# Performance work log

Measured on AMD Instinct MI355X. Metric: run time of the kernel, lower is better.

Reference implementation:

```python
import jax, jax.numpy as jnp
import numpy as np

N_NODES = 50000
N_EDGES = 1600000
N_FEAT = 256
HDIM = 64
HEADS = 8
N_GRAPHS = 64
NEG_SLOPE = 0.2


def gat_layer(x, src, dst, W, a_src, a_dst, b, heads, out_c, concat):
    # x: [N, F]; W: [F, heads*out_c]; a_src/a_dst: [heads, out_c]; b: bias
    N = x.shape[0]
    h = (x @ W).reshape(N, heads, out_c)              # [N, H, C]
    alpha_s = jnp.sum(h * a_src, axis=-1)             # [N, H]
    alpha_d = jnp.sum(h * a_dst, axis=-1)             # [N, H]
    e = jax.nn.leaky_relu(alpha_s[src] + alpha_d[dst], NEG_SLOPE)  # [E, H]
    # numerically stable segment softmax over incoming edges of each dst node
    m = jax.lax.stop_gradient(jax.ops.segment_max(e, dst, num_segments=N))
    p = jnp.exp(e - m[dst])
    denom = jax.ops.segment_sum(p, dst, num_segments=N)
    alpha = p / denom[dst]                            # [E, H]
    out = jax.ops.segment_sum(h[src] * alpha[:, :, None], dst, num_segments=N)  # [N, H, C]
    out = out.reshape(N, heads * out_c) if concat else out.mean(axis=1)
    return out + b


def setup_inputs() -> dict:
    key = jax.random.key(0)
    ks = jax.random.split(key, 10)
    x = jax.random.normal(ks[0], (N_NODES, N_FEAT), dtype=jnp.float32)
    edge_index = jax.random.randint(ks[1], (2, N_EDGES), 0, N_NODES, dtype=jnp.int64)
    batch = jnp.sort(jax.random.randint(ks[2], (N_NODES,), 0, N_GRAPHS, dtype=jnp.int64))
    c1 = HDIM // HEADS  # 8 channels per head
    s1 = 1.0 / np.sqrt(N_FEAT)
    s2 = 1.0 / np.sqrt(HDIM)
    W1 = jax.random.normal(ks[3], (N_FEAT, HEADS * c1), dtype=jnp.float32) * s1
    a_src1 = jax.random.normal(ks[4], (HEADS, c1), dtype=jnp.float32) * s2
    a_dst1 = jax.random.normal(ks[5], (HEADS, c1), dtype=jnp.float32) * s2
    b1 = jnp.zeros((HEADS * c1,), dtype=jnp.float32)
    W2 = jax.random.normal(ks[6], (HDIM, 1), dtype=jnp.float32) * s2
    a_src2 = jax.random.normal(ks[7], (1, 1), dtype=jnp.float32)
    a_dst2 = jax.random.normal(ks[8], (1, 1), dtype=jnp.float32)
    b2 = jnp.zeros((1,), dtype=jnp.float32)
    return {"x": x, "edge_index": edge_index, "batch": batch,
            "W1": W1, "a_src1": a_src1, "a_dst1": a_dst1, "b1": b1,
            "W2": W2, "a_src2": a_src2, "a_dst2": a_dst2, "b2": b2}


def reference(x, edge_index, batch, W1, a_src1, a_dst1, b1, W2, a_src2, a_dst2, b2):
    N = x.shape[0]
    # PyG GATConv adds self-loops by default
    loops = jnp.arange(N, dtype=edge_index.dtype)
    src = jnp.concatenate([edge_index[0], loops])
    dst = jnp.concatenate([edge_index[1], loops])
    c1 = HDIM // HEADS
    h = gat_layer(x, src, dst, W1, a_src1, a_dst1, b1, HEADS, c1, concat=True)
    h = jax.nn.relu(h)
    # dropout is identity in eval mode (training=False)
    h = gat_layer(h, src, dst, W2, a_src2, a_dst2, b2, 1, 1, concat=False)  # [N, 1]
    # global mean pool over graphs
    counts = jax.ops.segment_sum(jnp.ones((N,), dtype=h.dtype), batch, num_segments=N_GRAPHS)
    sums = jax.ops.segment_sum(h, batch, num_segments=N_GRAPHS)  # [G, 1]
    return sums / jnp.maximum(counts, 1.0)[:, None]
```

## Files before the change

### kernel.cpp

```cpp
#include <hip/hip_runtime.h>
#include <hip/hip_bf16.h>
#include <hip/hip_fp16.h>
#include <math.h>

#define NF 256
#define NO 64
#define NHEAD 8
#define NEG_SLOPE 0.2f
#define BM 64
#define KB 64
#define LS 68
#define BKT 128
#define NBLK 256
#define RCAP 8192

__device__ __forceinline__ float lrelu(float x) { return x > 0.f ? x : NEG_SLOPE * x; }

__global__ __launch_bounds__(256) void k_front(
    const float* __restrict__ x, const float* __restrict__ W,
    const float* __restrict__ a_src, const float* __restrict__ a_dst,
    __half* __restrict__ h1h, float* __restrict__ as1, float* __restrict__ ad1,
    const int* __restrict__ eidx, unsigned* __restrict__ M,
    float* __restrict__ gacc, int N, int E, int GB, int NB, int CH)
{
    __shared__ float xl[BM][LS];
    __shared__ float wl[KB][LS];

    if (blockIdx.x >= GB) {
        unsigned* hist = (unsigned*)&xl[0][0];
        for (int i = threadIdx.x; i < NB; i += 256) hist[i] = 0;
        __syncthreads();
        const int blk = blockIdx.x - GB;
        const int lo = blk * CH;
        const int hi = min(lo + CH, E + N);
        for (int i = lo + (int)threadIdx.x; i < hi; i += 256) {
            int d = (i < E) ? eidx[E + i] : (i - E);
            atomicAdd(&hist[d >> 7], 1u);
        }
        __syncthreads();
        for (int b = threadIdx.x; b < NB; b += 256)
            M[(size_t)b * NBLK + blk] = hist[b];
        return;
    }

    if (blockIdx.x == 0) {
        for (int i = threadIdx.x; i < 1024; i += 256) gacc[i] = 0.f;
    }
    const int t  = threadIdx.x;
    const int tx = t & 15;
    const int ty = t >> 4;
    const int row0 = blockIdx.x * BM;

    float acc[4][4] = {};

    for (int kc = 0; kc < NF; kc += KB) {
        #pragma unroll
        for (int i = 0; i < 4; ++i) {
            int r = (t >> 4) + 16 * i;
            int row = row0 + r; if (row >= N) row = N - 1;
            float4 v = *(const float4*)(x + (size_t)row * NF + kc + 4 * tx);
            *(float4*)&xl[r][4 * tx] = v;
        }
        #pragma unroll
        for (int i = 0; i < 4; ++i) {
            int k = (t >> 4) + 16 * i;
            float4 v = *(const float4*)(W + (size_t)(kc + k) * NO + 4 * tx);
            *(float4*)&wl[k][4 * tx] = v;
        }
        __syncthreads();

        #pragma unroll
        for (int k = 0; k < KB; k += 4) {
            float4 xv[4], wv[4];
            #pragma unroll
            for (int r = 0; r < 4; ++r)
                xv[r] = *(const float4*)&xl[4 * ty + r][k];
            #pragma unroll
            for (int kk = 0; kk < 4; ++kk)
                wv[kk] = *(const float4*)&wl[k + kk][4 * tx];
            #pragma unroll
            for (int r = 0; r < 4; ++r) {
                float4 xr = xv[r];
                #pragma unroll
                for (int kk = 0; kk < 4; ++kk) {
                    float xk = (kk == 0) ? xr.x : (kk == 1) ? xr.y : (kk == 2) ? xr.z : xr.w;
                    acc[r][0] = fmaf(xk, wv[kk].x, acc[r][0]);
                    acc[r][1] = fmaf(xk, wv[kk].y, acc[r][1]);
                    acc[r][2] = fmaf(xk, wv[kk].z, acc[r][2]);
                    acc[r][3] = fmaf(xk, wv[kk].w, acc[r][3]);
                }
            }
        }
        __syncthreads();
    }

    const float4 avs = *(const float4*)(a_src + 4 * tx);
    const float4 avd = *(const float4*)(a_dst + 4 * tx);
    #pragma unroll
    for (int r = 0; r < 4; ++r) {
        int row = row0 + 4 * ty + r;
        if (row >= N) continue;
        float4 o = make_float4(acc[r][0], acc[r][1], acc[r][2], acc[r][3]);
        __half2 p0 = __float22half2_rn(make_float2(o.x, o.y));
        __half2 p1 = __float22half2_rn(make_float2(o.z, o.w));
        __half2* dst2 = (__half2*)(h1h + (size_t)row * NO + 4 * tx);
        dst2[0] = p0;
        dst2[1] = p1;
        float vs = o.x * avs.x + o.y * avs.y + o.z * avs.z + o.w * avs.w;
        float vd = o.x * avd.x + o.y * avd.y + o.z * avd.z + o.w * avd.w;
        vs += __shfl_xor(vs, 1);
        vd += __shfl_xor(vd, 1);
        if ((tx & 1) == 0) {
            as1[row * NHEAD + (tx >> 1)] = vs;
            ad1[row * NHEAD + (tx >> 1)] = vd;
        }
    }
}

__global__ __launch_bounds__(1024) void k_scan2(
    unsigned* __restrict__ M, unsigned* __restrict__ Bbase, int NB)
{
    __shared__ unsigned tot[512];
    __shared__ unsigned basel[513];
    const int t = threadIdx.x, lane = t & 63, w = t >> 6;

    for (int b = w; b < NB; b += 16) {
        uint4 v = ((const uint4*)&M[(size_t)b * NBLK])[lane];
        unsigned s = v.x + v.y + v.z + v.w;
        #pragma unroll
        for (int m = 1; m < 64; m <<= 1) s += __shfl_xor(s, m);
        if (lane == 0) tot[b] = s;
    }
    __syncthreads();
    if (t == 0) {
        unsigned r = 0;
        for (int b = 0; b < NB; ++b) { basel[b] = r; r += tot[b]; }
        basel[NB] = r;
    }
    __syncthreads();
    for (int b = t; b <= NB; b += 1024) Bbase[b] = basel[b];
    for (int b = w; b < NB; b += 16) {
        uint4 v = ((const uint4*)&M[(size_t)b * NBLK])[lane];
        unsigned lsum = v.x + v.y + v.z + v.w;
        unsigned p = lsum;
        #pragma unroll
        for (int d = 1; d < 64; d <<= 1) {
            unsigned q = __shfl_up(p, d);
            if (lane >= d) p += q;
        }
        unsigned c0 = basel[b] + p - lsum;
        uint4 o;
        o.x = c0;
        o.y = c0 + v.x;
        o.z = o.y + v.y;
        o.w = o.z + v.z;
        ((uint4*)&M[(size_t)b * NBLK])[lane] = o;
    }
}

__global__ __launch_bounds__(256) void k_bscatter(
    const int* __restrict__ eidx, int E, int N, int NB, int CH,
    const unsigned* __restrict__ M, unsigned* __restrict__ rbuf)
{
    __shared__ unsigned cur[512];
    const int blk = blockIdx.x;
    for (int b = threadIdx.x; b < NB; b += 256)
        cur[b] = M[(size_t)b * NBLK + blk];
    __syncthreads();
    const int lo = blk * CH;
    const int hi = min(lo + CH, E + N);
    for (int i = lo + (int)threadIdx.x; i < hi; i += 256) {
        int s, d;
        if (i < E) { s = eidx[i]; d = eidx[E + i]; }
        else       { s = i - E;   d = i - E; }
        unsigned pos = atomicAdd(&cur[d >> 7], 1u);
        rbuf[pos] = ((unsigned)s << 7) | (unsigned)(d & (BKT - 1));
    }
}

__global__ __launch_bounds__(256) void k_csr(
    const unsigned* __restrict__ Bbase, int N, int NB,
    unsigned* __restrict__ rbuf, unsigned* __restrict__ offs)
{
    __shared__ unsigned recs[RCAP];
    __shared__ unsigned nhist[BKT];
    __shared__ unsigned ncur[BKT];
    __shared__ unsigned wtotS;
    const int b = blockIdx.x;
    const unsigned base = Bbase[b], end = Bbase[b + 1];
    const int cnt = (int)(end - base);
    const int nodes = min(BKT, N - b * BKT);

    for (int i = threadIdx.x; i < BKT; i += 256) nhist[i] = 0;
    __syncthreads();
    for (int i = threadIdx.x; i < cnt; i += 256) {
        unsigned r = rbuf[base + i];
        recs[i] = r;
        atomicAdd(&nhist[r & (BKT - 1)], 1u);
    }
    __syncthreads();
    const int tl = threadIdx.x & 127;
    unsigned v = nhist[tl], p = v;
    #pragma unroll
    for (int d = 1; d < 64; d <<= 1) {
        unsigned q = __shfl_up(p, d);
        if ((tl & 63) >= d) p += q;
    }
    if (threadIdx.x == 63) wtotS = p;
    __syncthreads();
    unsigned excl = base + ((tl >= 64) ? wtotS : 0u) + p - v;
    if (threadIdx.x < 128) {
        ncur[tl] = excl;
        if (tl < nodes) offs[b * BKT + tl] = excl;
    }
    if (b == NB - 1 && threadIdx.x == 0) offs[N] = end;
    __syncthreads();
    for (int i = threadIdx.x; i < cnt; i += 256) {
        unsigned r = recs[i];
        unsigned pos = atomicAdd(&ncur[r & (BKT - 1)], 1u);
        rbuf[pos] = r >> 7;
    }
}

__global__ __launch_bounds__(256) void k_gat1(
    const unsigned* __restrict__ offs, const int* __restrict__ csr,
    const float4* __restrict__ h1q,
    const float* __restrict__ as1, const float* __restrict__ ad1,
    const float* __restrict__ b1, const float* __restrict__ W2,
    float* __restrict__ h2, int N)
{
    const int lane = threadIdx.x & 63;
    const int n = blockIdx.x * (blockDim.x >> 6) + (threadIdx.x >> 6);
    if (n >= N) return;
    const int slot = lane >> 3;
    const int head = lane & 7;
    const unsigned s0 = offs[n];
    const unsigned deg = offs[n + 1] - s0;
    const float ad = ad1[n * NHEAD + head];

    float acc[8] = {};
    float den = 0.f;

    unsigned k = (unsigned)slot;
    for (; k + 24 < deg; k += 32) {
        int sA = csr[s0 + k],      sB = csr[s0 + k + 8];
        int sC = csr[s0 + k + 16], sD = csr[s0 + k + 24];
        float aA = as1[sA * NHEAD + head], aB = as1[sB * NHEAD + head];
        float aC = as1[sC * NHEAD + head], aD = as1[sD * NHEAD + head];
        float4 rA = h1q[(unsigned)sA * 8u + head];
        float4 rB = h1q[(unsigned)sB * 8u + head];
        float4 rC = h1q[(unsigned)sC * 8u + head];
        float4 rD = h1q[(unsigned)sD * 8u + head];
        float pA = __expf(lrelu(aA + ad));
        float pB = __expf(lrelu(aB + ad));
        float pC = __expf(lrelu(aC + ad));
        float pD = __expf(lrelu(aD + ad));
        den += (pA + pB) + (pC + pD);
        const __half2* hA = (const __half2*)&rA;
        const __half2* hB = (const __half2*)&rB;
        const __half2* hC = (const __half2*)&rC;
        const __half2* hD = (const __half2*)&rD;
        #pragma unroll
        for (int j = 0; j < 4; ++j) {
            float2 fA = __half22float2(hA[j]);
            float2 fB = __half22float2(hB[j]);
            float2 fC = __half22float2(hC[j]);
            float2 fD = __half22float2(hD[j]);
            acc[2 * j]     = fmaf(pA, fA.x, acc[2 * j]);
            acc[2 * j + 1] = fmaf(pA, fA.y, acc[2 * j + 1]);
            acc[2 * j]     = fmaf(pB, fB.x, acc[2 * j]);
            acc[2 * j + 1] = fmaf(pB, fB.y, acc[2 * j + 1]);
            acc[2 * j]     = fmaf(pC, fC.x, acc[2 * j]);
            acc[2 * j + 1] = fmaf(pC, fC.y, acc[2 * j + 1]);
            acc[2 * j]     = fmaf(pD, fD.x, acc[2 * j]);
            acc[2 * j + 1] = fmaf(pD, fD.y, acc[2 * j + 1]);
        }
    }
    for (; k + 8 < deg; k += 16) {
        int sA = csr[s0 + k], sB = csr[s0 + k + 8];
        float aA = as1[sA * NHEAD + head], aB = as1[sB * NHEAD + head];
        float4 rA = h1q[(unsigned)sA * 8u + head];
        float4 rB = h1q[(unsigned)sB * 8u + head];
        float pA = __expf(lrelu(aA + ad));
        float pB = __expf(lrelu(aB + ad));
        den += pA + pB;
        const __half2* hA = (const __half2*)&rA;
        const __half2* hB = (const __half2*)&rB;
        #pragma unroll
        for (int j = 0; j < 4; ++j) {
            float2 fA = __half22float2(hA[j]);
            float2 fB = __half22float2(hB[j]);
            acc[2 * j]     = fmaf(pA, fA.x, acc[2 * j]);
            acc[2 * j + 1] = fmaf(pA, fA.y, acc[2 * j + 1]);
            acc[2 * j]     = fmaf(pB, fB.x, acc[2 * j]);
            acc[2 * j + 1] = fmaf(pB, fB.y, acc[2 * j + 1]);
        }
    }
    if (k < deg) {
        int s = csr[s0 + k];
        float a = as1[s * NHEAD + head];
        float4 r = h1q[(unsigned)s * 8u + head];
        float p = __expf(lrelu(a + ad));
        den += p;
        const __half2* hh = (const __half2*)&r;
        #pragma unroll
        for (int j = 0; j < 4; ++j) {
            float2 f = __half22float2(hh[j]);
            acc[2 * j]     = fmaf(p, f.x, acc[2 * j]);
            acc[2 * j + 1] = fmaf(p, f.y, acc[2 * j + 1]);
        }
    }

    #pragma unroll
    for (int r = 0; r < 8; ++r) {
        acc[r] += __shfl_xor(acc[r], 8);
        acc[r] += __shfl_xor(acc[r], 16);
        acc[r] += __shfl_xor(acc[r], 32);
    }
    den += __shfl_xor(den, 8);
    den += __shfl_xor(den, 16);
    den += __shfl_xor(den, 32);

    const float4 b0 = ((const float4*)b1)[head * 2];
    const float4 b1v = ((const float4*)b1)[head * 2 + 1];
    const float4 w0 = ((const float4*)W2)[head * 2];
    const float4 w1v = ((const float4*)W2)[head * 2 + 1];
    const float inv = 1.f / den;
    float tt = 0.f;
    tt += fmaxf(fmaf(acc[0], inv, b0.x), 0.f) * w0.x;
    tt += fmaxf(fmaf(acc[1], inv, b0.y), 0.f) * w0.y;
    tt += fmaxf(fmaf(acc[2], inv, b0.z), 0.f) * w0.z;
    tt += fmaxf(fmaf(acc[3], inv, b0.w), 0.f) * w0.w;
    tt += fmaxf(fmaf(acc[4], inv, b1v.x), 0.f) * w1v.x;
    tt += fmaxf(fmaf(acc[5], inv, b1v.y), 0.f) * w1v.y;
    tt += fmaxf(fmaf(acc[6], inv, b1v.z), 0.f) * w1v.z;
    tt += fmaxf(fmaf(acc[7], inv, b1v.w), 0.f) * w1v.w;
    tt += __shfl_xor(tt, 1);
    tt += __shfl_xor(tt, 2);
    tt += __shfl_xor(tt, 4);
    if (lane == 0) h2[n] = tt;
}

__global__ __launch_bounds__(1024) void k_gat2pool(
    const unsigned* __restrict__ offs, const int* __restrict__ csr,
    const float* __restrict__ h2, const int* __restrict__ batch,
    const float* __restrict__ a_src2, const float* __restrict__ a_dst2,
    const float* __restrict__ b2, float* __restrict__ gacc, int N)
{
    __shared__ float vals[64];
    __shared__ int gid[64];
    const int t = threadIdx.x;
    if (t < 64) gid[t] = -1;
    __syncthreads();

    const int lane = t & 63;
    const int ql = lane & 15;
    const int slot = (t >> 6) * 4 + (lane >> 4);
    const int n = blockIdx.x * 64 + slot;

    if (n < N) {
        const float aS = a_src2[0], aD = a_dst2[0];
        const unsigned s0 = offs[n], s1 = offs[n + 1];
        const float ad = h2[n] * aD;
        float num = 0.f, den = 0.f;
        for (unsigned j = s0 + (unsigned)ql; j < s1; j += 16) {
            float hs = h2[csr[j]];
            float p = __expf(lrelu(hs * aS + ad));
            num = fmaf(p, hs, num);
            den += p;
        }
        #pragma unroll
        for (int msk = 1; msk < 16; msk <<= 1) {
            num += __shfl_xor(num, msk);
            den += __shfl_xor(den, msk);
        }
        if (ql == 0) {
            vals[slot] = num / den + b2[0];
            gid[slot] = batch[n];
        }
    }
    __syncthreads();

    if (t < 64) {
        int g = gid[t];
        float o = (g >= 0) ? vals[t] : 0.f;
        const int g0 = __shfl(g, 0);
        const bool same = (g == g0);
        float s = same ? o : 0.f;
        float c = (same && g >= 0) ? 1.f : 0.f;
        #pragma unroll
        for (int msk = 1; msk < 64; msk <<= 1) {
            s += __shfl_xor(s, msk);
            c += __shfl_xor(c, msk);
        }
        if (t == 0) {
            unsafeAtomicAdd(&gacc[g0 * 16], s);
            unsafeAtomicAdd(&gacc[g0 * 16 + 1], c);
        }
        if (g >= 0 && !same) {
            unsafeAtomicAdd(&gacc[g * 16], o);
            unsafeAtomicAdd(&gacc[g * 16 + 1], 1.0f);
        }
    }
}

__global__ void k_final(const float* __restrict__ gacc,
                        float* __restrict__ out, int G)
{
    int g = blockIdx.x * blockDim.x + threadIdx.x;
    if (g < G) out[g] = gacc[g * 16] / fmaxf(gacc[g * 16 + 1], 1.0f);
}

extern "C" void kernel_launch(void* const* d_in, const int* in_sizes, int n_in,
                              void* d_out, int out_size, void* d_ws, size_t ws_size,
                              hipStream_t stream)
{
    const float* x      = (const float*)d_in[0];
    const int*   eidx   = (const int*)d_in[1];
    const int*   batch  = (const int*)d_in[2];
    const float* W1     = (const float*)d_in[3];
    const float* a_src1 = (const float*)d_in[4];
    const float* a_dst1 = (const float*)d_in[5];
    const float* b1     = (const float*)d_in[6];
    const float* W2     = (const float*)d_in[7];
    const float* a_src2 = (const float*)d_in[8];
    const float* a_dst2 = (const float*)d_in[9];
    const float* b2     = (const float*)d_in[10];

    const int N = in_sizes[0] / NF;
    const int E = in_sizes[1] / 2;
    const int G = out_size;
    const int ETOT = E + N;
    const int NB = (N + BKT - 1) / BKT;
    const int CH = (ETOT + NBLK - 1) / NBLK;
    const int GB = (N + BM - 1) / BM;

    char* w = (char*)d_ws;
    __half*   h1h   = (__half*)(w + 0);
    float*    as1   = (float*)(w + 6400000);
    float*    ad1   = (float*)(w + 8000000);
    float*    h2    = (float*)(w + 9600000);
    unsigned* offs  = (unsigned*)(w + 9800000);
    unsigned* rbuf  = (unsigned*)(w + 10000064);
    unsigned* M     = (unsigned*)(w + 16600064);
    unsigned* Bbase = (unsigned*)(w + 17000448);
    float*    gacc  = (float*)(w + 17002496);

    k_front<<<GB + NBLK, 256, 0, stream>>>(x, W1, a_src1, a_dst1,
                                           h1h, as1, ad1,
                                           eidx, M, gacc, N, E, GB, NB, CH);
    k_scan2<<<1, 1024, 0, stream>>>(M, Bbase, NB);
    k_bscatter<<<NBLK, 256, 0, stream>>>(eidx, E, N, NB, CH, M, rbuf);
    k_csr<<<NB, 256, 0, stream>>>(Bbase, N, NB, rbuf, offs);

    const int* csr = (const int*)rbuf;
    k_gat1<<<(N + 3) / 4, 256, 0, stream>>>(offs, csr, (const float4*)h1h,
                                            as1, ad1, b1, W2, h2, N);
    k_gat2pool<<<(N + 63) / 64, 1024, 0, stream>>>(offs, csr, h2, batch,
                                                   a_src2, a_dst2, b2, gacc, N);
    k_final<<<1, 64, 0, stream>>>(gacc, (float*)d_out, G);
}
```

Before: 145.2 us.

## Use fp16 packed dot2 GEMM with register-prefetched tiles in front kernel

The x@W projection now converts x and W tiles to packed fp16 pairs in shared memory and accumulates with the fdot2 instruction in fp32, halving LDS traffic and FMA count. Global loads for the next K chunk are prefetched into registers while the current chunk is staged, overlapping memory latency with compute. Rounding inputs to fp16 lowers GEMM precision. The histogram scratch also moves into its own shared array.

```diff
diff --git a/kernel.cpp b/kernel.cpp
--- a/kernel.cpp
+++ b/kernel.cpp
@@ -9,12 +9,27 @@
 #define NEG_SLOPE 0.2f
 #define BM 64
 #define KB 64
-#define LS 68
 #define BKT 128
 #define NBLK 256
 #define RCAP 8192
 
 __device__ __forceinline__ float lrelu(float x) { return x > 0.f ? x : NEG_SLOPE * x; }
+
+typedef _Float16 f16x2 __attribute__((ext_vector_type(2)));
+
+__device__ __forceinline__ unsigned f2u(float a, float b) {
+    return __builtin_bit_cast(unsigned, __float22half2_rn(make_float2(a, b)));
+}
+__device__ __forceinline__ float dot2f(unsigned a, unsigned b, float c) {
+#if __has_builtin(__builtin_amdgcn_fdot2)
+    return __builtin_amdgcn_fdot2(__builtin_bit_cast(f16x2, a),
+                                  __builtin_bit_cast(f16x2, b), c, false);
+#else
+    float2 fa = __half22float2(__builtin_bit_cast(__half2, a));
+    float2 fb = __half22float2(__builtin_bit_cast(__half2, b));
+    return fmaf(fa.x, fb.x, fmaf(fa.y, fb.y, c));
+#endif
+}
 
 __global__ __launch_bounds__(256) void k_front(
     const float* __restrict__ x, const float* __restrict__ W,
@@ -23,11 +38,11 @@
     const int* __restrict__ eidx, unsigned* __restrict__ M,
     float* __restrict__ gacc, int N, int E, int GB, int NB, int CH)
 {
-    __shared__ float xl[BM][LS];
-    __shared__ float wl[KB][LS];
+    __shared__ unsigned xl2[BM][36];
+    __shared__ unsigned wl2[KB / 2][68];
+    __shared__ unsigned hist[512];
 
     if (blockIdx.x >= GB) {
-        unsigned* hist = (unsigned*)&xl[0][0];
         for (int i = threadIdx.x; i < NB; i += 256) hist[i] = 0;
         __syncthreads();
         const int blk = blockIdx.x - GB;
@@ -52,46 +67,73 @@
     const int row0 = blockIdx.x * BM;
 
     float acc[4][4] = {};
+    float4 xr[4], wr[4];
+
+    #pragma unroll
+    for (int i = 0; i < 4; ++i) {
+        int row = row0 + ty + 16 * i; if (row >= N) row = N - 1;
+        xr[i] = *(const float4*)(x + (size_t)row * NF + 4 * tx);
+    }
+    #pragma unroll
+    for (int i = 0; i < 2; ++i) {
+        int p = ty + 16 * i;
+        wr[2 * i]     = *(const float4*)(W + (size_t)(2 * p) * NO + 4 * tx);
+        wr[2 * i + 1] = *(const float4*)(W + (size_t)(2 * p + 1) * NO + 4 * tx);
+    }
 
     for (int kc = 0; kc < NF; kc += KB) {
+        __syncthreads();
         #pragma unroll
         for (int i = 0; i < 4; ++i) {
-            int r = (t >> 4) + 16 * i;
-            int row = row0 + r; if (row >= N) row = N - 1;
-            float4 v = *(const float4*)(x + (size_t)row * NF + kc + 4 * tx);
-            *(float4*)&xl[r][4 * tx] = v;
-        }
-        #pragma unroll
-        for (int i = 0; i < 4; ++i) {
-            int k = (t >> 4) + 16 * i;
-            float4 v = *(const float4*)(W + (size_t)(kc + k) * NO + 4 * tx);
-            *(float4*)&wl[k][4 * tx] = v;
+            int r = ty + 16 * i;
+            *(uint2*)&xl2[r][2 * tx] =
+                make_uint2(f2u(xr[i].x, xr[i].y), f2u(xr[i].z, xr[i].w));
+        }
+        #pragma unroll
+        for (int i = 0; i < 2; ++i) {
+            int p = ty + 16 * i;
+            float4 lo = wr[2 * i], hi = wr[2 * i + 1];
+            *(uint4*)&wl2[p][4 * tx] =
+                make_uint4(f2u(lo.x, hi.x), f2u(lo.y, hi.y),
+                           f2u(lo.z, hi.z), f2u(lo.w, hi.w));
+        }
+        if (kc + KB < NF) {
+            const int kn = kc + KB;
+            #pragma unroll
+            for (int i = 0; i < 4; ++i) {
+                int row = row0 + ty + 16 * i; if (row >= N) row = N - 1;
+                xr[i] = *(const float4*)(x + (size_t)row * NF + kn + 4 * tx);
+            }
+            #pragma unroll
+            for (int i = 0; i < 2; ++i) {
+                int p = ty + 16 * i;
+                wr[2 * i]     = *(const float4*)(W + (size_t)(kn + 2 * p) * NO + 4 * tx);
+                wr[2 * i + 1] = *(const float4*)(W + (size_t)(kn + 2 * p + 1) * NO + 4 * tx);
+            }
         }
         __syncthreads();
-
-        #pragma unroll
-        for (int k = 0; k < KB; k += 4) {
-            float4 xv[4], wv[4];
+        #pragma unroll
+        for (int kk = 0; kk < KB / 2; kk += 4) {
+            uint4 xv[4], wv[4];
             #pragma unroll
             for (int r = 0; r < 4; ++r)
-                xv[r] = *(const float4*)&xl[4 * ty + r][k];
+                xv[r] = *(const uint4*)&xl2[4 * ty + r][kk];
             #pragma unroll
-            for (int kk = 0; kk < 4; ++kk)
-                wv[kk] = *(const float4*)&wl[k + kk][4 * tx];
+            for (int j = 0; j < 4; ++j)
+                wv[j] = *(const uint4*)&wl2[kk + j][4 * tx];
             #pragma unroll
             for (int r = 0; r < 4; ++r) {
-                float4 xr = xv[r];
                 #pragma unroll
-                for (int kk = 0; kk < 4; ++kk) {
-                    float xk = (kk == 0) ? xr.x : (kk == 1) ? xr.y : (kk == 2) ? xr.z : xr.w;
-                    acc[r][0] = fmaf(xk, wv[kk].x, acc[r][0]);
-                    acc[r][1] = fmaf(xk, wv[kk].y, acc[r][1]);
-                    acc[r][2] = fmaf(xk, wv[kk].z, acc[r][2]);
-                    acc[r][3] = fmaf(xk, wv[kk].w, acc[r][3]);
+                for (int j = 0; j < 4; ++j) {
+                    unsigned xa = (j == 0) ? xv[r].x : (j == 1) ? xv[r].y
+                                : (j == 2) ? xv[r].z : xv[r].w;
+                    acc[r][0] = dot2f(xa, wv[j].x, acc[r][0]);
+                    acc[r][1] = dot2f(xa, wv[j].y, acc[r][1]);
+                    acc[r][2] = dot2f(xa, wv[j].z, acc[r][2]);
+                    acc[r][3] = dot2f(xa, wv[j].w, acc[r][3]);
                 }
             }
         }
-        __syncthreads();
     }
 
     const float4 avs = *(const float4*)(a_src + 4 * tx);
```

New measurement: 494.6 us. 241% more time.

## Compute first-layer projection with fp16 MFMA instead of fp32 FMA

Applied to the files above, without the earlier changes.

The x@W1 GEMM in k_front moves from a scalar fp32 register-tiled FMA loop to 16x16x32 f16 MFMA instructions. x and W are converted to packed half2 in shared memory, and W is stored transposed. The K tile grows to 128, and the epilogue computes the attention logits per head with lane shuffles over the MFMA output layout. The goal is to cut the GEMM's compute time, at the cost of fp16 input precision and scalar, non-vectorized stores of h1h.

```diff
diff --git a/kernel.cpp b/kernel.cpp
--- a/kernel.cpp
+++ b/kernel.cpp
@@ -7,14 +7,19 @@
 #define NO 64
 #define NHEAD 8
 #define NEG_SLOPE 0.2f
-#define BM 64
-#define KB 64
-#define LS 68
 #define BKT 128
 #define NBLK 256
 #define RCAP 8192
 
 __device__ __forceinline__ float lrelu(float x) { return x > 0.f ? x : NEG_SLOPE * x; }
+
+typedef _Float16 f16x8 __attribute__((ext_vector_type(8)));
+typedef float f32x4 __attribute__((ext_vector_type(4)));
+
+__device__ __forceinline__ unsigned f2u(float a, float b) {
+    __half2 h = __float22half2_rn(make_float2(a, b));
+    return *(unsigned*)&h;
+}
 
 __global__ __launch_bounds__(256) void k_front(
     const float* __restrict__ x, const float* __restrict__ W,
@@ -23,11 +28,11 @@
     const int* __restrict__ eidx, unsigned* __restrict__ M,
     float* __restrict__ gacc, int N, int E, int GB, int NB, int CH)
 {
-    __shared__ float xl[BM][LS];
-    __shared__ float wl[KB][LS];
+    __shared__ unsigned xl2[64][68];
+    __shared__ unsigned wl2[64][68];
 
     if (blockIdx.x >= GB) {
-        unsigned* hist = (unsigned*)&xl[0][0];
+        unsigned* hist = &xl2[0][0];
         for (int i = threadIdx.x; i < NB; i += 256) hist[i] = 0;
         __syncthreads();
         const int blk = blockIdx.x - GB;
@@ -46,73 +51,72 @@
     if (blockIdx.x == 0) {
         for (int i = threadIdx.x; i < 1024; i += 256) gacc[i] = 0.f;
     }
-    const int t  = threadIdx.x;
-    const int tx = t & 15;
-    const int ty = t >> 4;
-    const int row0 = blockIdx.x * BM;
-
-    float acc[4][4] = {};
-
-    for (int kc = 0; kc < NF; kc += KB) {
-        #pragma unroll
-        for (int i = 0; i < 4; ++i) {
-            int r = (t >> 4) + 16 * i;
+    const int t   = threadIdx.x;
+    const int lw  = t & 63;
+    const int wv  = t >> 6;
+    const int row0 = blockIdx.x * 64;
+
+    f32x4 acc[4] = {};
+
+    for (int kc = 0; kc < NF; kc += 128) {
+        if (kc) __syncthreads();
+        {
+            const int r = t >> 2, q = t & 3;
             int row = row0 + r; if (row >= N) row = N - 1;
-            float4 v = *(const float4*)(x + (size_t)row * NF + kc + 4 * tx);
-            *(float4*)&xl[r][4 * tx] = v;
-        }
-        #pragma unroll
-        for (int i = 0; i < 4; ++i) {
-            int k = (t >> 4) + 16 * i;
-            float4 v = *(const float4*)(W + (size_t)(kc + k) * NO + 4 * tx);
-            *(float4*)&wl[k][4 * tx] = v;
+            const float4* xs = (const float4*)(x + (size_t)row * NF + kc + q * 32);
+            #pragma unroll
+            for (int i = 0; i < 8; ++i) {
+                float4 v = xs[i];
+                xl2[r][q * 16 + 2 * i]     = f2u(v.x, v.y);
+                xl2[r][q * 16 + 2 * i + 1] = f2u(v.z, v.w);
+            }
+        }
+        {
+            const int c = t & 63, seg = t >> 6;
+            #pragma unroll
+            for (int m = 0; m < 16; ++m) {
+                int k = kc + seg * 32 + 2 * m;
+                float w0 = W[(size_t)k * NO + c];
+                float w1 = W[(size_t)(k + 1) * NO + c];
+                wl2[c][seg * 16 + m] = f2u(w0, w1);
+            }
         }
         __syncthreads();
 
-        #pragma unroll
-        for (int k = 0; k < KB; k += 4) {
-            float4 xv[4], wv[4];
+        const int mrow = 16 * wv + (lw & 15);
+        const int fcol = (lw >> 4) * 4;
+        #pragma unroll
+        for (int ks = 0; ks < 4; ++ks) {
+            f16x8 a = *(const f16x8*)&xl2[mrow][ks * 16 + fcol];
             #pragma unroll
-            for (int r = 0; r < 4; ++r)
-                xv[r] = *(const float4*)&xl[4 * ty + r][k];
-            #pragma unroll
-            for (int kk = 0; kk < 4; ++kk)
-                wv[kk] = *(const float4*)&wl[k + kk][4 * tx];
-            #pragma unroll
-            for (int r = 0; r < 4; ++r) {
-                float4 xr = xv[r];
-                #pragma unroll
-                for (int kk = 0; kk < 4; ++kk) {
-                    float xk = (kk == 0) ? xr.x : (kk == 1) ? xr.y : (kk == 2) ? xr.z : xr.w;
-                    acc[r][0] = fmaf(xk, wv[kk].x, acc[r][0]);
-                    acc[r][1] = fmaf(xk, wv[kk].y, acc[r][1]);
-                    acc[r][2] = fmaf(xk, wv[kk].z, acc[r][2]);
-                    acc[r][3] = fmaf(xk, wv[kk].w, acc[r][3]);
+            for (int ct = 0; ct < 4; ++ct) {
+                f16x8 b = *(const f16x8*)&wl2[16 * ct + (lw & 15)][ks * 16 + fcol];
+                acc[ct] = __builtin_amdgcn_mfma_f32_16x16x32_f16(a, b, acc[ct], 0, 0, 0);
+            }
+        }
+    }
+
+    const int colb = lw & 15;
+    #pragma unroll
+    for (int ct = 0; ct < 4; ++ct) {
+        const int col = 16 * ct + colb;
+        const float asc = a_src[col];
+        const float adc = a_dst[col];
+        #pragma unroll
+        for (int j = 0; j < 4; ++j) {
+            const int rowAbs = row0 + 16 * wv + (lw >> 4) * 4 + j;
+            float v = acc[ct][j];
+            float vs = v * asc, vd = v * adc;
+            vs += __shfl_xor(vs, 1); vs += __shfl_xor(vs, 2); vs += __shfl_xor(vs, 4);
+            vd += __shfl_xor(vd, 1); vd += __shfl_xor(vd, 2); vd += __shfl_xor(vd, 4);
+            if (rowAbs < N) {
+                h1h[(size_t)rowAbs * NO + col] = __float2half(v);
+                if ((colb & 7) == 0) {
+                    int head = 2 * ct + (colb >> 3);
+                    as1[rowAbs * NHEAD + head] = vs;
+                    ad1[rowAbs * NHEAD + head] = vd;
                 }
             }
-        }
-        __syncthreads();
-    }
-
-    const float4 avs = *(const float4*)(a_src + 4 * tx);
-    const float4 avd = *(const float4*)(a_dst + 4 * tx);
-    #pragma unroll
-    for (int r = 0; r < 4; ++r) {
-        int row = row0 + 4 * ty + r;
-        if (row >= N) continue;
-        float4 o = make_float4(acc[r][0], acc[r][1], acc[r][2], acc[r][3]);
-        __half2 p0 = __float22half2_rn(make_float2(o.x, o.y));
-        __half2 p1 = __float22half2_rn(make_float2(o.z, o.w));
-        __half2* dst2 = (__half2*)(h1h + (size_t)row * NO + 4 * tx);
-        dst2[0] = p0;
-        dst2[1] = p1;
-        float vs = o.x * avs.x + o.y * avs.y + o.z * avs.z + o.w * avs.w;
-        float vd = o.x * avd.x + o.y * avd.y + o.z * avd.z + o.w * avd.w;
-        vs += __shfl_xor(vs, 1);
-        vd += __shfl_xor(vd, 1);
-        if ((tx & 1) == 0) {
-            as1[row * NHEAD + (tx >> 1)] = vs;
-            ad1[row * NHEAD + (tx >> 1)] = vd;
         }
     }
 }
@@ -433,7 +437,7 @@
     const int ETOT = E + N;
     const int NB = (N + BKT - 1) / BKT;
     const int CH = (ETOT + NBLK - 1) / NBLK;
-    const int GB = (N + BM - 1) / BM;
+    const int GB = (N + 63) / 64;
 
     char* w = (char*)d_ws;
     __half*   h1h   = (__half*)(w + 0);
```

After: 132.5 us. -8.8%, faster.
